# Optimization experiments

Hardware: AMD Instinct MI355X
Metric: run time of the kernel (lower is better)

The kernel has to match this reference:

```python
import jax, jax.numpy as jnp
import numpy as np

B, T, D, UNITS, NUM_OUT = 64, 1024, 256, 256, 32


def setup_inputs() -> dict:
    key = jax.random.key(0)
    k1, k2, k3 = jax.random.split(key, 3)
    inputs = jax.random.normal(k1, (B, T, D), dtype=jnp.float32)
    U = jax.random.normal(k2, (D, 4 * UNITS), dtype=jnp.float32) * 0.05
    W = jax.random.normal(k3, (UNITS, 4 * UNITS), dtype=jnp.float32) * 0.05
    b = jnp.zeros((4 * UNITS,), dtype=jnp.float32)
    return {"inputs": inputs, "U": U, "W": W, "b": b, "num_outputs": NUM_OUT}


def reference(inputs, U, W, b, num_outputs):
    # inputs: [B, T, D]; U: [D, 4u]; W: [u, 4u]; b: [4u]
    Bsz, Tlen, _ = inputs.shape
    units = W.shape[0]
    # Precompute input projection as one batched GEMM (x_t @ U + b for all t)
    xz = jnp.einsum('btd,dk->btk', inputs, U) + b  # [B, T, 4u]

    def step(carry, xz_t):
        h, c = carry
        z = xz_t + h @ W  # [B, 4u]
        z0, z1, z2, z3 = jnp.split(z, 4, axis=1)
        i = jax.nn.sigmoid(z0)
        f = jax.nn.sigmoid(z1)
        c_new = f * c + i * jnp.tanh(z2)
        o = jax.nn.sigmoid(z3)
        h_new = o * jnp.tanh(c_new)
        return (h_new, c_new), h_new

    h0 = jnp.zeros((Bsz, units), dtype=inputs.dtype)
    c0 = jnp.zeros((Bsz, units), dtype=inputs.dtype)
    (_, _), hs = jax.lax.scan(step, (h0, c0), jnp.swapaxes(xz, 0, 1))  # hs: [T, B, u]
    outputs = jnp.swapaxes(hs, 0, 1)[:, Tlen - num_outputs:, :]  # [B, num_outputs, u]
    return outputs
```

## Files before the change

kernel.cpp:

```cpp
#include <hip/hip_runtime.h>
#include <hip/hip_fp16.h>
#include <stdint.h>

#define Bsz 64
#define Tsz 1024
#define Dsz 256
#define UNITSn 256
#define Zdim 1024
#define NWV 6
#define NWL 2


typedef _Float16 half2v __attribute__((ext_vector_type(2)));

__device__ __forceinline__ float dot2acc(uint32_t w, uint32_t h, float acc) {
#if __has_builtin(__builtin_amdgcn_fdot2)
  return __builtin_amdgcn_fdot2(__builtin_bit_cast(half2v, w),
                                __builtin_bit_cast(half2v, h), acc, false);
#else
  __half2 wv = __builtin_bit_cast(__half2, w);
  __half2 hv = __builtin_bit_cast(__half2, h);
  acc = fmaf(__half2float(__low2half(wv)),  __half2float(__low2half(hv)),  acc);
  acc = fmaf(__half2float(__high2half(wv)), __half2float(__high2half(hv)), acc);
  return acc;
#endif
}

__device__ __forceinline__ float dot4(const uint4& w, const uint4& h, float acc) {
  acc = dot2acc(w.x, h.x, acc); acc = dot2acc(w.y, h.y, acc);
  acc = dot2acc(w.z, h.z, acc); acc = dot2acc(w.w, h.w, acc);
  return acc;
}

__device__ __forceinline__ float sigm(float x)   { return 1.0f / (1.0f + __expf(-x)); }
__device__ __forceinline__ float tanh_f(float x) { return 1.0f - 2.0f / (__expf(2.0f * x) + 1.0f); }

__global__ __launch_bounds__(256) void convert_w4(const float* __restrict__ W,
                                                  uint4* __restrict__ WregBuf,
                                                  uint4* __restrict__ WldsBuf) {
  int i = blockIdx.x * 256 + threadIdx.x;
  if (i >= 32768) return;
  bool isReg = i < NWV * 4 * 1024;
  int t, g, k2rel, outIdx;
  if (isReg) {
    int cI = i >> 10; t = i & 1023;
    g = cI / NWV; int j = cI - g * NWV;
    k2rel = j * 4;
    outIdx = i;
  } else {
    int i2 = i - NWV * 4 * 1024;
    int cI = i2 >> 10; t = i2 & 1023;
    g = cI >> 1; int jj = cI & 1;
    k2rel = NWV * 4 + jj * 4;
    outIdx = i2;
  }
  int col = g * 256 + (t & 255);
  int kbase = (t >> 8) * 32 + k2rel;
  uint32_t d[4];
#pragma unroll
  for (int e = 0; e < 4; e++) {
    int k2 = kbase + e;
    float w0 = W[(size_t)(2 * k2) * Zdim + col];
    float w1 = W[(size_t)(2 * k2 + 1) * Zdim + col];
    __half2 p = __floats2half2_rn(w0, w1);
    d[e] = __builtin_bit_cast(uint32_t, p);
  }
  uint4 v = make_uint4(d[0], d[1], d[2], d[3]);
  if (isReg) WregBuf[outIdx] = v;
  else       WldsBuf[outIdx] = v;
}

__global__ __launch_bounds__(256) void proj_gemm(
    const float* __restrict__ x, const float* __restrict__ U,
    const float* __restrict__ bias, float* __restrict__ xz, int t0) {
  __shared__ float At[32][68];
  __shared__ float Bt[32][68];
  const int tid  = threadIdx.x;
  const int n0   = blockIdx.x * 64;
  const int tloc = blockIdx.y;
  const int t    = t0 + tloc;
  const int tm = tid >> 4, tn = tid & 15;
  const int am = tid >> 3, ak = (tid & 7) * 4;
  const int bk = tid >> 4, bn = (tid & 15) * 4;
  const float* xb = x + (size_t)t * Dsz;

  float acc[4][4] = {};
  for (int k0 = 0; k0 < Dsz; k0 += 32) {
    float4 a0 = *(const float4*)(xb + (size_t)am * (Tsz * Dsz) + k0 + ak);
    float4 a1 = *(const float4*)(xb + (size_t)(am + 32) * (Tsz * Dsz) + k0 + ak);
    float4 b0 = *(const float4*)(U + (size_t)(k0 + bk) * Zdim + n0 + bn);
    float4 b1 = *(const float4*)(U + (size_t)(k0 + bk + 16) * Zdim + n0 + bn);
    __syncthreads();
    At[ak + 0][am] = a0.x; At[ak + 1][am] = a0.y; At[ak + 2][am] = a0.z; At[ak + 3][am] = a0.w;
    At[ak + 0][am + 32] = a1.x; At[ak + 1][am + 32] = a1.y; At[ak + 2][am + 32] = a1.z; At[ak + 3][am + 32] = a1.w;
    *(float4*)&Bt[bk][bn]      = b0;
    *(float4*)&Bt[bk + 16][bn] = b1;
    __syncthreads();
#pragma unroll
    for (int kk = 0; kk < 32; kk++) {
      float4 av = *(const float4*)&At[kk][tm * 4];
      float4 bv = *(const float4*)&Bt[kk][tn * 4];
      float a_[4] = {av.x, av.y, av.z, av.w};
      float b_[4] = {bv.x, bv.y, bv.z, bv.w};
#pragma unroll
      for (int i = 0; i < 4; i++)
#pragma unroll
        for (int j = 0; j < 4; j++) acc[i][j] = fmaf(a_[i], b_[j], acc[i][j]);
    }
  }
  float4 bb = *(const float4*)&bias[n0 + tn * 4];
  float bias_[4] = {bb.x, bb.y, bb.z, bb.w};
#pragma unroll
  for (int i = 0; i < 4; i++) {
    float4 o;
    o.x = acc[i][0] + bias_[0]; o.y = acc[i][1] + bias_[1];
    o.z = acc[i][2] + bias_[2]; o.w = acc[i][3] + bias_[3];
    *(float4*)(xz + ((size_t)tloc * 64 + tm * 4 + i) * Zdim + n0 + tn * 4) = o;
  }
}

__global__ __launch_bounds__(1024) void lstm_chunk(
    const float* __restrict__ xz, const uint4* __restrict__ WregBuf,
    const uint4* __restrict__ WldsBuf, float* __restrict__ out,
    uint4* __restrict__ h_state, float* __restrict__ c_state,
    int t0, int Tc, int n_out) {
  extern __shared__ uint4 smem4[];
  uint4* Wl   = smem4;
  uint4* hq   = smem4 + 8192;
  float4* pp  = (float4*)(smem4 + 8192 + 64);

  const int tid = threadIdx.x;
  const int b   = blockIdx.x;
  const int q   = tid >> 8, u = tid & 255;

  uint4 wr[4][NWV];
#pragma unroll
  for (int g = 0; g < 4; g++)
#pragma unroll
    for (int j = 0; j < NWV; j++)
      wr[g][j] = WregBuf[(size_t)(g * NWV + j) * 1024 + tid];
#pragma unroll
  for (int cc = 0; cc < 4 * NWL; cc++)
    Wl[(size_t)cc * 1024 + tid] = WldsBuf[(size_t)cc * 1024 + tid];

  float c = 0.0f;
  if (t0 == 0) {
    if (tid < 64) hq[tid] = make_uint4(0, 0, 0, 0);
  } else {
    if (tid < 32) hq[tid] = h_state[(size_t)b * 32 + tid];
    if (q == 0)   c = c_state[(size_t)b * 256 + u];
  }
  __syncthreads();

  const float* xzb = xz + (size_t)b * Zdim + u;
  float nx0 = 0, nx1 = 0, nx2 = 0, nx3 = 0;
  if (q == 0) { nx0 = xzb[0]; nx1 = xzb[256]; nx2 = xzb[512]; nx3 = xzb[768]; }

  for (int tl = 0; tl < Tc; tl++) {
    const int buf = tl & 1;
    const uint4* hb = hq + buf * 32 + q * 8;
    float a0 = 0, a1 = 0, a2 = 0, a3 = 0;
#pragma unroll
    for (int cj = 0; cj < NWL; cj++) {
      uint4 h4 = hb[NWV + cj];
      uint4 w0 = Wl[(size_t)(0 * NWL + cj) * 1024 + tid];
      uint4 w1 = Wl[(size_t)(1 * NWL + cj) * 1024 + tid];
      uint4 w2 = Wl[(size_t)(2 * NWL + cj) * 1024 + tid];
      uint4 w3 = Wl[(size_t)(3 * NWL + cj) * 1024 + tid];
      a0 = dot4(w0, h4, a0); a1 = dot4(w1, h4, a1);
      a2 = dot4(w2, h4, a2); a3 = dot4(w3, h4, a3);
    }
#pragma unroll
    for (int j = 0; j < NWV; j++) {
      uint4 h4 = hb[j];
      a0 = dot4(wr[0][j], h4, a0);
      a1 = dot4(wr[1][j], h4, a1);
      a2 = dot4(wr[2][j], h4, a2);
      a3 = dot4(wr[3][j], h4, a3);
    }
    if (q) pp[(size_t)(q - 1) * 256 + u] = make_float4(a0, a1, a2, a3);
    __syncthreads();
    if (!q) {
      float4 p0 = pp[u], p1 = pp[256 + u], p2 = pp[512 + u];
      float z0 = a0 + p0.x + p1.x + p2.x + nx0;
      float z1 = a1 + p0.y + p1.y + p2.y + nx1;
      float z2 = a2 + p0.z + p1.z + p2.z + nx2;
      float z3 = a3 + p0.w + p1.w + p2.w + nx3;
      if (tl + 1 < Tc) {
        const float* xn = xzb + (size_t)(tl + 1) * (Bsz * Zdim);
        nx0 = xn[0]; nx1 = xn[256]; nx2 = xn[512]; nx3 = xn[768];
      }
      float ig = sigm(z0), fg = sigm(z1), gg = tanh_f(z2), og = sigm(z3);
      c = fg * c + ig * gg;
      float hn = og * tanh_f(c);
      int ot = (t0 + tl) - (Tsz - n_out);
      if (ot >= 0) out[((size_t)b * n_out + ot) * UNITSn + u] = hn;
      ((__half*)(hq + (buf ^ 1) * 32))[u] = __float2half(hn);
    }
    __syncthreads();
  }
  if (tid < 32) h_state[(size_t)b * 32 + tid] = hq[(Tc & 1) * 32 + tid];
  if (q == 0)   c_state[(size_t)b * 256 + u] = c;
}

extern "C" void kernel_launch(void* const* d_in, const int* in_sizes, int n_in,
                              void* d_out, int out_size, void* d_ws, size_t ws_size,
                              hipStream_t stream) {
  const float* x    = (const float*)d_in[0];
  const float* U    = (const float*)d_in[1];
  const float* W    = (const float*)d_in[2];
  const float* bias = (const float*)d_in[3];
  float* out = (float*)d_out;
  const int n_out = out_size / (Bsz * UNITSn);

  uint8_t* ws = (uint8_t*)d_ws;
  uint4* WregBuf = (uint4*)ws;
  uint4* WldsBuf = (uint4*)(ws + (384u << 10));
  uint4* h_state = (uint4*)(ws + (512u << 10));
  float* c_state = (float*)(ws + (544u << 10));
  float* xz      = (float*)(ws + (1u << 20));

  int Tc = Tsz;
  while (Tc > 1 && (size_t)(1u << 20) + (size_t)Tc * (Bsz * Zdim) * 4 > ws_size) Tc >>= 1;

  convert_w4<<<dim3(128), dim3(256), 0, stream>>>(W, WregBuf, WldsBuf);

  const int ldsBytes = (8192 + 64 + 768) * 16;
  hipFuncSetAttribute((const void*)lstm_chunk,
                      hipFuncAttributeMaxDynamicSharedMemorySize, ldsBytes);

  for (int t0 = 0; t0 < Tsz; t0 += Tc) {
    proj_gemm<<<dim3(16, Tc), dim3(256), 0, stream>>>(x, U, bias, xz, t0);
    lstm_chunk<<<dim3(Bsz), dim3(1024), ldsBytes, stream>>>(xz, WregBuf, WldsBuf,
                                                            out, h_state, c_state,
                                                            t0, Tc, n_out);
  }
}
```

Baseline: 2.082 ms.

## Use MFMA fp16 for input projection and halve LSTM block to 512 threads

The input projection GEMM is rewritten to use fp16 MFMA 16x16x32 instructions on a pre-transposed fp16 copy of U instead of scalar FP32 FMAs. The recurrent kernel drops from 1024 to 512 threads per block, so each thread covers twice the K range. Its weights are split three ways: registers, LDS, and a slice streamed from global/L2 every step with double-buffered prefetch. This cuts the cross-wave reduction to one partial sum and raises per-thread work, at the cost of streaming part of W from cache each timestep and rounding x and U to fp16 in the projection.

Measured after the change: 1.813 ms. 12.9% less time.

```diff
diff --git a/kernel.cpp b/kernel.cpp
--- a/kernel.cpp
+++ b/kernel.cpp
@@ -7,11 +7,10 @@
 #define Dsz 256
 #define UNITSn 256
 #define Zdim 1024
-#define NWV 6
-#define NWL 2
-
 
 typedef _Float16 half2v __attribute__((ext_vector_type(2)));
+typedef _Float16 f16x8  __attribute__((ext_vector_type(8)));
+typedef float    f32x4  __attribute__((ext_vector_type(4)));
 
 __device__ __forceinline__ float dot2acc(uint32_t w, uint32_t h, float acc) {
 #if __has_builtin(__builtin_amdgcn_fdot2)
@@ -35,27 +34,33 @@
 __device__ __forceinline__ float sigm(float x)   { return 1.0f / (1.0f + __expf(-x)); }
 __device__ __forceinline__ float tanh_f(float x) { return 1.0f - 2.0f / (__expf(2.0f * x) + 1.0f); }
 
-__global__ __launch_bounds__(256) void convert_w4(const float* __restrict__ W,
-                                                  uint4* __restrict__ WregBuf,
-                                                  uint4* __restrict__ WldsBuf) {
+__global__ __launch_bounds__(256) void convert_u(const float* __restrict__ U,
+                                                 _Float16* __restrict__ UT) {
+  int i = blockIdx.x * 256 + threadIdx.x;
+  int n = i >> 8, k = i & 255;
+  UT[i] = (_Float16)U[(size_t)k * Zdim + n];
+}
+
+__global__ __launch_bounds__(256) void convert_w5(const float* __restrict__ W,
+                                                  uint4* __restrict__ Wop,
+                                                  uint4* __restrict__ Wlds,
+                                                  uint4* __restrict__ Wstr) {
   int i = blockIdx.x * 256 + threadIdx.x;
   if (i >= 32768) return;
-  bool isReg = i < NWV * 4 * 1024;
-  int t, g, k2rel, outIdx;
-  if (isReg) {
-    int cI = i >> 10; t = i & 1023;
-    g = cI / NWV; int j = cI - g * NWV;
-    k2rel = j * 4;
-    outIdx = i;
+  int t, g, k2base, outIdx;
+  uint4* dst;
+  if (i < 8192) {
+    int j = i >> 9; t = i & 511; g = j & 3; k2base = (j >> 2) * 4;
+    dst = Wop; outIdx = i;
+  } else if (i < 14336) {
+    int i2 = i - 8192; int cl = i2 >> 9; t = i2 & 511; g = cl & 3;
+    k2base = 16 + (cl >> 2) * 4; dst = Wlds; outIdx = i2;
   } else {
-    int i2 = i - NWV * 4 * 1024;
-    int cI = i2 >> 10; t = i2 & 1023;
-    g = cI >> 1; int jj = cI & 1;
-    k2rel = NWV * 4 + jj * 4;
-    outIdx = i2;
+    int i3 = i - 14336; int kb = i3 >> 11; int r = i3 & 2047;
+    t = r >> 2; g = r & 3; k2base = 28 + kb * 4; dst = Wstr; outIdx = i3;
   }
   int col = g * 256 + (t & 255);
-  int kbase = (t >> 8) * 32 + k2rel;
+  int kbase = (t >> 8) * 64 + k2base;
   uint32_t d[4];
 #pragma unroll
   for (int e = 0; e < 4; e++) {
@@ -65,127 +70,161 @@
     __half2 p = __floats2half2_rn(w0, w1);
     d[e] = __builtin_bit_cast(uint32_t, p);
   }
-  uint4 v = make_uint4(d[0], d[1], d[2], d[3]);
-  if (isReg) WregBuf[outIdx] = v;
-  else       WldsBuf[outIdx] = v;
-}
-
-__global__ __launch_bounds__(256) void proj_gemm(
-    const float* __restrict__ x, const float* __restrict__ U,
+  dst[outIdx] = make_uint4(d[0], d[1], d[2], d[3]);
+}
+
+__global__ __launch_bounds__(256) void proj_mfma(
+    const float* __restrict__ x, const _Float16* __restrict__ UT,
     const float* __restrict__ bias, float* __restrict__ xz, int t0) {
-  __shared__ float At[32][68];
-  __shared__ float Bt[32][68];
+  __shared__ _Float16 Ax[64][40];
+  __shared__ _Float16 Ux[256][40];
   const int tid  = threadIdx.x;
-  const int n0   = blockIdx.x * 64;
+  const int w    = tid >> 6, lane = tid & 63;
+  const int lr   = lane & 15, kg = lane >> 4;
+  const int n0   = blockIdx.x * 256;
   const int tloc = blockIdx.y;
   const int t    = t0 + tloc;
-  const int tm = tid >> 4, tn = tid & 15;
-  const int am = tid >> 3, ak = (tid & 7) * 4;
-  const int bk = tid >> 4, bn = (tid & 15) * 4;
-  const float* xb = x + (size_t)t * Dsz;
-
-  float acc[4][4] = {};
+  const int arow = tid >> 2, ak = (tid & 3) * 8;
+
+  f32x4 acc[4][4];
+#pragma unroll
+  for (int mi = 0; mi < 4; mi++)
+#pragma unroll
+    for (int ni = 0; ni < 4; ni++) acc[mi][ni] = f32x4{0.f, 0.f, 0.f, 0.f};
+
   for (int k0 = 0; k0 < Dsz; k0 += 32) {
-    float4 a0 = *(const float4*)(xb + (size_t)am * (Tsz * Dsz) + k0 + ak);
-    float4 a1 = *(const float4*)(xb + (size_t)(am + 32) * (Tsz * Dsz) + k0 + ak);
-    float4 b0 = *(const float4*)(U + (size_t)(k0 + bk) * Zdim + n0 + bn);
-    float4 b1 = *(const float4*)(U + (size_t)(k0 + bk + 16) * Zdim + n0 + bn);
-    __syncthreads();
-    At[ak + 0][am] = a0.x; At[ak + 1][am] = a0.y; At[ak + 2][am] = a0.z; At[ak + 3][am] = a0.w;
-    At[ak + 0][am + 32] = a1.x; At[ak + 1][am + 32] = a1.y; At[ak + 2][am + 32] = a1.z; At[ak + 3][am + 32] = a1.w;
-    *(float4*)&Bt[bk][bn]      = b0;
-    *(float4*)&Bt[bk + 16][bn] = b1;
-    __syncthreads();
-#pragma unroll
-    for (int kk = 0; kk < 32; kk++) {
-      float4 av = *(const float4*)&At[kk][tm * 4];
-      float4 bv = *(const float4*)&Bt[kk][tn * 4];
-      float a_[4] = {av.x, av.y, av.z, av.w};
-      float b_[4] = {bv.x, bv.y, bv.z, bv.w};
-#pragma unroll
-      for (int i = 0; i < 4; i++)
-#pragma unroll
-        for (int j = 0; j < 4; j++) acc[i][j] = fmaf(a_[i], b_[j], acc[i][j]);
+    const float* xp = x + ((size_t)arow * Tsz + t) * Dsz + k0 + ak;
+    float4 p0 = *(const float4*)xp;
+    float4 p1 = *(const float4*)(xp + 4);
+    const _Float16* up = UT + (size_t)(n0 + tid) * Dsz + k0;
+    f16x8 u0 = *(const f16x8*)up;
+    f16x8 u1 = *(const f16x8*)(up + 8);
+    f16x8 u2 = *(const f16x8*)(up + 16);
+    f16x8 u3 = *(const f16x8*)(up + 24);
+    __syncthreads();
+    f16x8 a8;
+    a8[0] = (_Float16)p0.x; a8[1] = (_Float16)p0.y;
+    a8[2] = (_Float16)p0.z; a8[3] = (_Float16)p0.w;
+    a8[4] = (_Float16)p1.x; a8[5] = (_Float16)p1.y;
+    a8[6] = (_Float16)p1.z; a8[7] = (_Float16)p1.w;
+    *(f16x8*)&Ax[arow][ak] = a8;
+    *(f16x8*)&Ux[tid][0]  = u0;
+    *(f16x8*)&Ux[tid][8]  = u1;
+    *(f16x8*)&Ux[tid][16] = u2;
+    *(f16x8*)&Ux[tid][24] = u3;
+    __syncthreads();
+    f16x8 af[4], uf[4];
+#pragma unroll
+    for (int mi = 0; mi < 4; mi++) af[mi] = *(const f16x8*)&Ax[mi * 16 + lr][kg * 8];
+#pragma unroll
+    for (int ni = 0; ni < 4; ni++) uf[ni] = *(const f16x8*)&Ux[w * 64 + ni * 16 + lr][kg * 8];
+#pragma unroll
+    for (int mi = 0; mi < 4; mi++)
+#pragma unroll
+      for (int ni = 0; ni < 4; ni++)
+        acc[mi][ni] = __builtin_amdgcn_mfma_f32_16x16x32_f16(af[mi], uf[ni],
+                                                             acc[mi][ni], 0, 0, 0);
+  }
+#pragma unroll
+  for (int ni = 0; ni < 4; ni++) {
+    int col = n0 + w * 64 + ni * 16 + lr;
+    float bs = bias[col];
+#pragma unroll
+    for (int mi = 0; mi < 4; mi++) {
+      f32x4 v = acc[mi][ni];
+#pragma unroll
+      for (int r = 0; r < 4; r++) {
+        int brow = mi * 16 + kg * 4 + r;
+        xz[((size_t)tloc * 64 + brow) * Zdim + col] = v[r] + bs;
+      }
     }
   }
-  float4 bb = *(const float4*)&bias[n0 + tn * 4];
-  float bias_[4] = {bb.x, bb.y, bb.z, bb.w};
-#pragma unroll
-  for (int i = 0; i < 4; i++) {
-    float4 o;
-    o.x = acc[i][0] + bias_[0]; o.y = acc[i][1] + bias_[1];
-    o.z = acc[i][2] + bias_[2]; o.w = acc[i][3] + bias_[3];
-    *(float4*)(xz + ((size_t)tloc * 64 + tm * 4 + i) * Zdim + n0 + tn * 4) = o;
-  }
-}
-
-__global__ __launch_bounds__(1024) void lstm_chunk(
-    const float* __restrict__ xz, const uint4* __restrict__ WregBuf,
-    const uint4* __restrict__ WldsBuf, float* __restrict__ out,
-    uint4* __restrict__ h_state, float* __restrict__ c_state,
-    int t0, int Tc, int n_out) {
+}
+
+__global__ __launch_bounds__(512) void lstm_chunk(
+    const float* __restrict__ xz, const uint4* __restrict__ Wop,
+    const uint4* __restrict__ WldsBuf, const uint4* __restrict__ Wstr,
+    float* __restrict__ out, uint4* __restrict__ h_state,
+    float* __restrict__ c_state, int t0, int Tc, int n_out) {
   extern __shared__ uint4 smem4[];
-  uint4* Wl   = smem4;
-  uint4* hq   = smem4 + 8192;
-  float4* pp  = (float4*)(smem4 + 8192 + 64);
-
-  const int tid = threadIdx.x;
-  const int b   = blockIdx.x;
-  const int q   = tid >> 8, u = tid & 255;
-
-  uint4 wr[4][NWV];
-#pragma unroll
-  for (int g = 0; g < 4; g++)
-#pragma unroll
-    for (int j = 0; j < NWV; j++)
-      wr[g][j] = WregBuf[(size_t)(g * NWV + j) * 1024 + tid];
-#pragma unroll
-  for (int cc = 0; cc < 4 * NWL; cc++)
-    Wl[(size_t)cc * 1024 + tid] = WldsBuf[(size_t)cc * 1024 + tid];
+  uint4*  Wl = smem4;
+  uint4*  hq = smem4 + 6144;
+  float4* pp = (float4*)(smem4 + 6144 + 64);
+
+  const int tid  = threadIdx.x;
+  const int b    = blockIdx.x;
+  const int half = tid >> 8, u = tid & 255;
+
+  uint4 wop[16];
+#pragma unroll
+  for (int j = 0; j < 16; j++) wop[j] = Wop[(size_t)j * 512 + tid];
+#pragma unroll
+  for (int j = 0; j < 16; j++)
+    asm volatile("" : "+v"(wop[j].x), "+v"(wop[j].y), "+v"(wop[j].z), "+v"(wop[j].w));
+#pragma unroll
+  for (int cl = 0; cl < 12; cl++)
+    Wl[(size_t)cl * 512 + tid] = WldsBuf[(size_t)cl * 512 + tid];
 
   float c = 0.0f;
   if (t0 == 0) {
     if (tid < 64) hq[tid] = make_uint4(0, 0, 0, 0);
   } else {
     if (tid < 32) hq[tid] = h_state[(size_t)b * 32 + tid];
-    if (q == 0)   c = c_state[(size_t)b * 256 + u];
+    if (half == 0) c = c_state[(size_t)b * 256 + u];
   }
   __syncthreads();
 
   const float* xzb = xz + (size_t)b * Zdim + u;
   float nx0 = 0, nx1 = 0, nx2 = 0, nx3 = 0;
-  if (q == 0) { nx0 = xzb[0]; nx1 = xzb[256]; nx2 = xzb[512]; nx3 = xzb[768]; }
+  if (half == 0) { nx0 = xzb[0]; nx1 = xzb[256]; nx2 = xzb[512]; nx3 = xzb[768]; }
+  const uint4* wstr = Wstr + (size_t)tid * 4;
+
+#define LDB(s, kb) { const uint4* p_ = wstr + (size_t)(kb) * 2048; \
+    s[0] = p_[0]; s[1] = p_[1]; s[2] = p_[2]; s[3] = p_[3]; }
+#define USEB(s, hi) { uint4 h4_ = hb[hi]; \
+    a0 = dot4(s[0], h4_, a0); a1 = dot4(s[1], h4_, a1); \
+    a2 = dot4(s[2], h4_, a2); a3 = dot4(s[3], h4_, a3); }
+#define LDSPH(jj2) { uint4 h4_ = hb[4 + (jj2)]; \
+    uint4 w0_ = Wl[(size_t)((jj2) * 4 + 0) * 512 + tid]; \
+    uint4 w1_ = Wl[(size_t)((jj2) * 4 + 1) * 512 + tid]; \
+    uint4 w2_ = Wl[(size_t)((jj2) * 4 + 2) * 512 + tid]; \
+    uint4 w3_ = Wl[(size_t)((jj2) * 4 + 3) * 512 + tid]; \
+    a0 = dot4(w0_, h4_, a0); a1 = dot4(w1_, h4_, a1); \
+    a2 = dot4(w2_, h4_, a2); a3 = dot4(w3_, h4_, a3); }
 
   for (int tl = 0; tl < Tc; tl++) {
     const int buf = tl & 1;
-    const uint4* hb = hq + buf * 32 + q * 8;
+    const uint4* hb = hq + buf * 32 + half * 16;
     float a0 = 0, a1 = 0, a2 = 0, a3 = 0;
-#pragma unroll
-    for (int cj = 0; cj < NWL; cj++) {
-      uint4 h4 = hb[NWV + cj];
-      uint4 w0 = Wl[(size_t)(0 * NWL + cj) * 1024 + tid];
-      uint4 w1 = Wl[(size_t)(1 * NWL + cj) * 1024 + tid];
-      uint4 w2 = Wl[(size_t)(2 * NWL + cj) * 1024 + tid];
-      uint4 w3 = Wl[(size_t)(3 * NWL + cj) * 1024 + tid];
-      a0 = dot4(w0, h4, a0); a1 = dot4(w1, h4, a1);
-      a2 = dot4(w2, h4, a2); a3 = dot4(w3, h4, a3);
+    uint4 sA[4], sB[4];
+    LDB(sA, 0); LDB(sB, 1);
+#pragma unroll
+    for (int jj = 0; jj < 4; jj++) {
+      uint4 h4 = hb[jj];
+      a0 = dot4(wop[jj * 4 + 0], h4, a0);
+      a1 = dot4(wop[jj * 4 + 1], h4, a1);
+      a2 = dot4(wop[jj * 4 + 2], h4, a2);
+      a3 = dot4(wop[jj * 4 + 3], h4, a3);
     }
-#pragma unroll
-    for (int j = 0; j < NWV; j++) {
-      uint4 h4 = hb[j];
-      a0 = dot4(wr[0][j], h4, a0);
-      a1 = dot4(wr[1][j], h4, a1);
-      a2 = dot4(wr[2][j], h4, a2);
-      a3 = dot4(wr[3][j], h4, a3);
-    }
-    if (q) pp[(size_t)(q - 1) * 256 + u] = make_float4(a0, a1, a2, a3);
-    __syncthreads();
-    if (!q) {
-      float4 p0 = pp[u], p1 = pp[256 + u], p2 = pp[512 + u];
-      float z0 = a0 + p0.x + p1.x + p2.x + nx0;
-      float z1 = a1 + p0.y + p1.y + p2.y + nx1;
-      float z2 = a2 + p0.z + p1.z + p2.z + nx2;
-      float z3 = a3 + p0.w + p1.w + p2.w + nx3;
+    USEB(sA, 7);  LDB(sA, 2);
+    LDSPH(0);
+    USEB(sB, 8);  LDB(sB, 3);
+    LDSPH(1);
+    USEB(sA, 9);  LDB(sA, 4);
+    LDSPH(2);
+    USEB(sB, 10); LDB(sB, 5);
+    USEB(sA, 11); LDB(sA, 6);
+    USEB(sB, 12); LDB(sB, 7);
+    USEB(sA, 13); LDB(sA, 8);
+    USEB(sB, 14);
+    USEB(sA, 15);
+
+    if (half) pp[u] = make_float4(a0, a1, a2, a3);
+    __syncthreads();
+    if (!half) {
+      float4 q = pp[u];
+      float z0 = a0 + q.x + nx0, z1 = a1 + q.y + nx1;
+      float z2 = a2 + q.z + nx2, z3 = a3 + q.w + nx3;
       if (tl + 1 < Tc) {
         const float* xn = xzb + (size_t)(tl + 1) * (Bsz * Zdim);
         nx0 = xn[0]; nx1 = xn[256]; nx2 = xn[512]; nx3 = xn[768];
@@ -200,7 +239,10 @@
     __syncthreads();
   }
   if (tid < 32) h_state[(size_t)b * 32 + tid] = hq[(Tc & 1) * 32 + tid];
-  if (q == 0)   c_state[(size_t)b * 256 + u] = c;
+  if (half == 0) c_state[(size_t)b * 256 + u] = c;
+#undef LDB
+#undef USEB
+#undef LDSPH
 }
 
 extern "C" void kernel_launch(void* const* d_in, const int* in_sizes, int n_in,
@@ -214,25 +256,28 @@
   const int n_out = out_size / (Bsz * UNITSn);
 
   uint8_t* ws = (uint8_t*)d_ws;
-  uint4* WregBuf = (uint4*)ws;
-  uint4* WldsBuf = (uint4*)(ws + (384u << 10));
-  uint4* h_state = (uint4*)(ws + (512u << 10));
-  float* c_state = (float*)(ws + (544u << 10));
-  float* xz      = (float*)(ws + (1u << 20));
+  uint4* Wop      = (uint4*)ws;
+  uint4* Wlds     = (uint4*)(ws + (128u << 10));
+  uint4* Wstr     = (uint4*)(ws + (224u << 10));
+  _Float16* UT    = (_Float16*)(ws + (512u << 10));
+  uint4* h_state  = (uint4*)(ws + (1024u << 10));
+  float* c_state  = (float*)(ws + (1056u << 10));
+  float* xz       = (float*)(ws + (2u << 20));
 
   int Tc = Tsz;
-  while (Tc > 1 && (size_t)(1u << 20) + (size_t)Tc * (Bsz * Zdim) * 4 > ws_size) Tc >>= 1;
-
-  convert_w4<<<dim3(128), dim3(256), 0, stream>>>(W, WregBuf, WldsBuf);
-
-  const int ldsBytes = (8192 + 64 + 768) * 16;
+  while (Tc > 1 && (size_t)(2u << 20) + (size_t)Tc * (Bsz * Zdim) * 4 > ws_size) Tc >>= 1;
+
+  convert_w5<<<dim3(128), dim3(256), 0, stream>>>(W, Wop, Wlds, Wstr);
+  convert_u<<<dim3(1024), dim3(256), 0, stream>>>(U, UT);
+
+  const int ldsBytes = (6144 + 64 + 256) * 16;
   hipFuncSetAttribute((const void*)lstm_chunk,
                       hipFuncAttributeMaxDynamicSharedMemorySize, ldsBytes);
 
   for (int t0 = 0; t0 < Tsz; t0 += Tc) {
-    proj_gemm<<<dim3(16, Tc), dim3(256), 0, stream>>>(x, U, bias, xz, t0);
-    lstm_chunk<<<dim3(Bsz), dim3(1024), ldsBytes, stream>>>(xz, WregBuf, WldsBuf,
-                                                            out, h_state, c_state,
-                                                            t0, Tc, n_out);
-  }
-}
+    proj_mfma<<<dim3(4, Tc), dim3(256), 0, stream>>>(x, UT, bias, xz, t0);
+    lstm_chunk<<<dim3(Bsz), dim3(512), ldsBytes, stream>>>(xz, Wop, Wlds, Wstr,
+                                                           out, h_state, c_state,
+                                                           t0, Tc, n_out);
+  }
+}
```
